# Optimization experiments

Measured on AMD Instinct MI355X. Metric: run time of the kernel, lower is better.

Reference implementation:

```python
import jax, jax.numpy as jnp
import numpy as np

GROUP = 16  # quantization group size along in_features
EPS = 1e-5


def setup_inputs() -> dict:
    key = jax.random.key(0)
    ks = jax.random.split(key, 6)
    B, D, L, R = 16384, 1024, 18, 32
    x = jax.random.normal(ks[0], (B, D), dtype=jnp.float32)
    # 4-bit codes in [0,16); shifted by -8 at dequant time -> values in [-8,7]
    wq = jax.random.randint(ks[1], (L, D, D), 0, 16, dtype=jnp.int32)
    # per-group positive scales, small so dequantized weights are O(0.1)
    scales = jax.random.uniform(ks[2], (L, D, D // GROUP), dtype=jnp.float32) * 0.05 + 0.005
    bias = jax.random.normal(ks[3], (L, D), dtype=jnp.float32) * 0.02
    # LoRA weights are zero-init in the module; use small random values so the
    # low-rank path is numerically exercised
    lora_a = jax.random.normal(ks[4], (L, R, D), dtype=jnp.float32) * 0.02
    lora_b = jax.random.normal(ks[5], (L, D, R), dtype=jnp.float32) * 0.02
    ln_gamma = jnp.ones((5, D), dtype=jnp.float32)
    ln_beta = jnp.zeros((5, D), dtype=jnp.float32)
    return {"x": x, "wq": wq, "scales": scales, "bias": bias,
            "lora_a": lora_a, "lora_b": lora_b,
            "ln_gamma": ln_gamma, "ln_beta": ln_beta}


def _dequant(wq_i, sc_i):
    # wq_i: [out, in] int codes; sc_i: [out, in//GROUP]
    O, I = wq_i.shape
    q = wq_i.astype(jnp.float32) - 8.0
    w = q.reshape(O, I // GROUP, GROUP) * sc_i[:, :, None]
    return w.reshape(O, I)


def _qlora(x, wq_i, sc_i, b_i, a_i, bm_i):
    w = _dequant(wq_i, sc_i)                       # [out, in]
    base = x @ w.T + b_i                           # frozen 4-bit base path
    lora = (x @ a_i.T) @ bm_i.T                    # low-rank adapter path
    return base + lora


def _layernorm(x, g, b):
    m = jnp.mean(x, axis=-1, keepdims=True)
    v = jnp.mean(jnp.square(x - m), axis=-1, keepdims=True)
    return (x - m) * jax.lax.rsqrt(v + EPS) * g + b


def reference(x, wq, scales, bias, lora_a, lora_b, ln_gamma, ln_beta):
    h = x
    for j in range(6):  # 6 residual blocks, 3 QLoRA layers each
        i = 3 * j
        r = h
        h = jax.nn.relu(_qlora(h, wq[i], scales[i], bias[i], lora_a[i], lora_b[i]))
        h = jax.nn.relu(_qlora(h, wq[i + 1], scales[i + 1], bias[i + 1], lora_a[i + 1], lora_b[i + 1]))
        h = _qlora(h, wq[i + 2], scales[i + 2], bias[i + 2], lora_a[i + 2], lora_b[i + 2])
        h = h + r
        if j < 5:
            h = _layernorm(h, ln_gamma[j], ln_beta[j])
    return h
```

## Files before the change

### kernel.cpp

```cpp
#include <hip/hip_runtime.h>
#include <hip/hip_bf16.h>
#include <stdint.h>

using bf16 = __hip_bfloat16;
typedef __attribute__((ext_vector_type(8))) short bf16x8;
typedef __attribute__((ext_vector_type(8))) unsigned short u16x8;
typedef __attribute__((ext_vector_type(16))) float f32x16;

#define B_ROWS 16384
#define D_DIM  1024
#define NLAYER 18

__device__ inline void gload_lds16(const bf16* g, bf16* l) {
    __builtin_amdgcn_global_load_lds(
        (const __attribute__((address_space(1))) void*)g,
        (__attribute__((address_space(3))) void*)l, 16, 0, 0);
}

__device__ inline unsigned short f2bf_bits(float f) {
    bf16 h = __float2bfloat16(f);
    return *reinterpret_cast<unsigned short*>(&h);
}
__device__ inline float bfbits2f(unsigned short u) {
    unsigned int x = ((unsigned int)u) << 16;
    return __uint_as_float(x);
}
__device__ inline void split_bf(float v, unsigned short& hi, unsigned short& lo) {
    hi = f2bf_bits(v);
    float hf = bfbits2f(hi);
    lo = f2bf_bits(v - hf);
}

__global__ __launch_bounds__(256)
void build_weff(const int* __restrict__ wq, const float* __restrict__ scales,
                const float* __restrict__ lora_a, const float* __restrict__ lora_b,
                bf16* __restrict__ weff_h, bf16* __restrict__ weff_l)
{
    const int bb = blockIdx.x;
    const int l  = bb >> 7;
    const int o0 = (bb & 127) * 8;
    __shared__ float bsh[8][32];
    {
        const int oo = threadIdx.x >> 5, rr = threadIdx.x & 31;
        bsh[oo][rr] = lora_b[((size_t)l * 1024 + o0 + oo) * 32 + rr];
    }
    __syncthreads();

    const float* abase = lora_a + (size_t)l * 32 * 1024;
    const int i0 = threadIdx.x * 4;
    float acc[8][4] = {};
    #pragma unroll 4
    for (int r = 0; r < 32; ++r) {
        float4 av = *reinterpret_cast<const float4*>(abase + (size_t)r * 1024 + i0);
        #pragma unroll
        for (int o = 0; o < 8; ++o) {
            const float br = bsh[o][r];
            acc[o][0] += br * av.x; acc[o][1] += br * av.y;
            acc[o][2] += br * av.z; acc[o][3] += br * av.w;
        }
    }
    #pragma unroll
    for (int o = 0; o < 8; ++o) {
        const size_t row = (size_t)l * 1024 + o0 + o;
        int4 q = *reinterpret_cast<const int4*>(wq + row * 1024 + i0);
        const float sc = scales[row * 64 + (i0 >> 4)];
        float w0 = (q.x - 8) * sc + acc[o][0];
        float w1 = (q.y - 8) * sc + acc[o][1];
        float w2 = (q.z - 8) * sc + acc[o][2];
        float w3 = (q.w - 8) * sc + acc[o][3];
        ushort4 uh, ul;
        split_bf(w0, uh.x, ul.x); split_bf(w1, uh.y, ul.y);
        split_bf(w2, uh.z, ul.z); split_bf(w3, uh.w, ul.w);
        *reinterpret_cast<ushort4*>(weff_h + row * 1024 + i0) = uh;
        *reinterpret_cast<ushort4*>(weff_l + row * 1024 + i0) = ul;
    }
}

__global__ __launch_bounds__(256)
void cast_split(const float* __restrict__ x, bf16* __restrict__ yh, bf16* __restrict__ yl)
{
    size_t i = ((size_t)blockIdx.x * 256 + threadIdx.x) * 4;
    float4 v = *reinterpret_cast<const float4*>(x + i);
    ushort4 uh, ul;
    split_bf(v.x, uh.x, ul.x); split_bf(v.y, uh.y, ul.y);
    split_bf(v.z, uh.z, ul.z); split_bf(v.w, uh.w, ul.w);
    *reinterpret_cast<ushort4*>(yh + i) = uh;
    *reinterpret_cast<ushort4*>(yl + i) = ul;
}

#define TILE_E 8192
#define SET_E  (4 * TILE_E)

#define SCHED0 __builtin_amdgcn_sched_barrier(0)

template<int MODE>
__global__ __launch_bounds__(512)
void qgemm3(const bf16* __restrict__ AH, const bf16* __restrict__ AL,
            const bf16* __restrict__ WH, const bf16* __restrict__ WL,
            const float* __restrict__ bias,
            const bf16* __restrict__ RH, const bf16* __restrict__ RL,
            bf16* __restrict__ OH, bf16* __restrict__ OL,
            float* __restrict__ Of)
{
    __shared__ bf16 smem[2 * SET_E];

    const int b  = blockIdx.x;
    const int sb = ((b & 7) << 5) | (b >> 3);
    const int n0 = (sb & 3) * 256;
    const int m0 = (sb >> 2) * 256;

    const int tid  = threadIdx.x;
    const int wave = tid >> 6;
    const int lane = tid & 63;
    const int wr = wave >> 2;
    const int wc = wave & 3;

    const int rl = lane >> 2;
    const int ps = lane & 3;
    const int l31 = lane & 31;
    const int khalf = lane >> 5;

    f32x16 acc[4][2] = {};

    auto stage = [&](int buf, int k0) {
        bf16* base = smem + buf * SET_E;
        #pragma unroll
        for (int t = 0; t < 2; ++t) {
            int s = wave * 2 + t;
            int r = s * 16 + rl;
            int q = ps ^ (r & 3) ^ ((r >> 2) & 3);
            size_t ga = (size_t)(m0 + r) * D_DIM + k0 + q * 8;
            size_t gb = (size_t)(n0 + r) * D_DIM + k0 + q * 8;
            bf16* dst = base + s * 512;
            gload_lds16(AH + ga, dst);
            gload_lds16(AL + ga, dst + TILE_E);
            gload_lds16(WH + gb, dst + 2 * TILE_E);
            gload_lds16(WL + gb, dst + 3 * TILE_E);
        }
    };

    stage(0, 0);

    #pragma unroll 1
    for (int kt = 0; kt < 32; ++kt) {
        const int cur = kt & 1;
        SCHED0;
        asm volatile("s_waitcnt vmcnt(0)" ::: "memory");
        SCHED0;
        __builtin_amdgcn_s_barrier();
        if (kt < 31)
            stage(cur ^ 1, (kt + 1) * 32);
        SCHED0;

        const bf16* tb = smem + cur * SET_E;
        bf16x8 wh[2][2], wl[2][2], ah[4][2], al[4][2];
        #pragma unroll
        for (int nt = 0; nt < 2; ++nt)
            #pragma unroll
            for (int kc = 0; kc < 2; ++kc) {
                int R = wc * 64 + nt * 32 + l31;
                int sl = kc * 2 + khalf;
                int p = sl ^ (R & 3) ^ ((R >> 2) & 3);
                int off = R * 32 + p * 8;
                wh[nt][kc] = *reinterpret_cast<const bf16x8*>(tb + 2 * TILE_E + off);
                wl[nt][kc] = *reinterpret_cast<const bf16x8*>(tb + 3 * TILE_E + off);
            }
        #pragma unroll
        for (int mt = 0; mt < 4; ++mt)
            #pragma unroll
            for (int kc = 0; kc < 2; ++kc) {
                int R = wr * 128 + mt * 32 + l31;
                int sl = kc * 2 + khalf;
                int p = sl ^ (R & 3) ^ ((R >> 2) & 3);
                int off = R * 32 + p * 8;
                ah[mt][kc] = *reinterpret_cast<const bf16x8*>(tb + off);
                al[mt][kc] = *reinterpret_cast<const bf16x8*>(tb + TILE_E + off);
            }

        __builtin_amdgcn_s_setprio(1);
        #pragma unroll
        for (int mt = 0; mt < 4; ++mt)
            #pragma unroll
            for (int nt = 0; nt < 2; ++nt)
                #pragma unroll
                for (int kc = 0; kc < 2; ++kc) {
                    acc[mt][nt] = __builtin_amdgcn_mfma_f32_32x32x16_bf16(ah[mt][kc], wh[nt][kc], acc[mt][nt], 0, 0, 0);
                    acc[mt][nt] = __builtin_amdgcn_mfma_f32_32x32x16_bf16(ah[mt][kc], wl[nt][kc], acc[mt][nt], 0, 0, 0);
                    acc[mt][nt] = __builtin_amdgcn_mfma_f32_32x32x16_bf16(al[mt][kc], wh[nt][kc], acc[mt][nt], 0, 0, 0);
                }
        __builtin_amdgcn_s_setprio(0);
    }

    SCHED0;
    asm volatile("s_waitcnt lgkmcnt(0)" ::: "memory");
    SCHED0;
    __builtin_amdgcn_s_barrier();

    float* cwave = reinterpret_cast<float*>(smem) + wave * 4096;
    const int rbase = 4 * khalf;
    const int rloc = lane >> 3;
    const int cloc = (lane & 7) * 8;

    #pragma unroll
    for (int half = 0; half < 2; ++half) {
        #pragma unroll
        for (int nt = 0; nt < 2; ++nt) {
            const float bv = bias[n0 + wc * 64 + nt * 32 + l31];
            const int lcol = nt * 32 + l31;
            const int chunk = lcol >> 2;
            #pragma unroll
            for (int mm = 0; mm < 2; ++mm) {
                const int mt = half * 2 + mm;
                #pragma unroll
                for (int reg = 0; reg < 16; ++reg) {
                    const int row32 = (reg & 3) + 8 * (reg >> 2) + rbase;
                    const int lrow = mm * 32 + row32;
                    float v = acc[mt][nt][reg] + bv;
                    if (MODE == 0) v = v > 0.f ? v : 0.f;
                    cwave[lrow * 64 + (chunk ^ (lrow & 15)) * 4 + (lcol & 3)] = v;
                }
            }
        }
        SCHED0;
        asm volatile("s_waitcnt lgkmcnt(0)" ::: "memory");
        SCHED0;

        #pragma unroll
        for (int pass = 0; pass < 8; ++pass) {
            const int lrow = pass * 8 + rloc;
            const int grow = m0 + wr * 128 + half * 64 + lrow;
            const size_t gbase = (size_t)grow * D_DIM + (n0 + wc * 64 + cloc);
            const int c0 = cloc >> 2;
            float4 v0 = *reinterpret_cast<const float4*>(&cwave[lrow * 64 + ((c0    ) ^ (lrow & 15)) * 4]);
            float4 v1 = *reinterpret_cast<const float4*>(&cwave[lrow * 64 + ((c0 + 1) ^ (lrow & 15)) * 4]);
            float vv[8] = {v0.x, v0.y, v0.z, v0.w, v1.x, v1.y, v1.z, v1.w};
            if (MODE != 0) {
                u16x8 rh = *reinterpret_cast<const u16x8*>(&RH[gbase]);
                u16x8 rl2 = *reinterpret_cast<const u16x8*>(&RL[gbase]);
                #pragma unroll
                for (int k = 0; k < 8; ++k)
                    vv[k] += bfbits2f(rh[k]) + bfbits2f(rl2[k]);
            }
            if (MODE == 2) {
                *reinterpret_cast<float4*>(&Of[gbase])     = make_float4(vv[0], vv[1], vv[2], vv[3]);
                *reinterpret_cast<float4*>(&Of[gbase + 4]) = make_float4(vv[4], vv[5], vv[6], vv[7]);
            } else {
                u16x8 ho, lo2;
                #pragma unroll
                for (int k = 0; k < 8; ++k) {
                    unsigned short h, l2;
                    split_bf(vv[k], h, l2);
                    ho[k] = h; lo2[k] = l2;
                }
                *reinterpret_cast<u16x8*>(&OH[gbase]) = ho;
                *reinterpret_cast<u16x8*>(&OL[gbase]) = lo2;
            }
        }
        SCHED0;
        asm volatile("s_waitcnt lgkmcnt(0)" ::: "memory");
        SCHED0;
    }
}

__global__ __launch_bounds__(256)
void ln_pair(const bf16* __restrict__ XH, const bf16* __restrict__ XL,
             bf16* __restrict__ YH, bf16* __restrict__ YL,
             const float* __restrict__ gamma, const float* __restrict__ beta)
{
    const int row = blockIdx.x;
    const int tid = threadIdx.x;
    const int lane = tid & 63;
    const int wave = tid >> 6;

    ushort4 uh = reinterpret_cast<const ushort4*>(XH + (size_t)row * D_DIM)[tid];
    ushort4 ul = reinterpret_cast<const ushort4*>(XL + (size_t)row * D_DIM)[tid];
    float v0 = bfbits2f(uh.x) + bfbits2f(ul.x);
    float v1 = bfbits2f(uh.y) + bfbits2f(ul.y);
    float v2 = bfbits2f(uh.z) + bfbits2f(ul.z);
    float v3 = bfbits2f(uh.w) + bfbits2f(ul.w);
    float s  = v0 + v1 + v2 + v3;
    float ss = v0 * v0 + v1 * v1 + v2 * v2 + v3 * v3;
    #pragma unroll
    for (int off = 32; off >= 1; off >>= 1) {
        s  += __shfl_xor(s, off, 64);
        ss += __shfl_xor(ss, off, 64);
    }
    __shared__ float red[8];
    if (lane == 0) { red[wave] = s; red[4 + wave] = ss; }
    __syncthreads();
    float S  = red[0] + red[1] + red[2] + red[3];
    float SS = red[4] + red[5] + red[6] + red[7];
    const float mean = S * (1.0f / D_DIM);
    const float var  = SS * (1.0f / D_DIM) - mean * mean;
    const float inv  = rsqrtf(var + 1e-5f);

    const int c0 = tid * 4;
    float y0 = (v0 - mean) * inv * gamma[c0 + 0] + beta[c0 + 0];
    float y1 = (v1 - mean) * inv * gamma[c0 + 1] + beta[c0 + 1];
    float y2 = (v2 - mean) * inv * gamma[c0 + 2] + beta[c0 + 2];
    float y3 = (v3 - mean) * inv * gamma[c0 + 3] + beta[c0 + 3];
    ushort4 oh, ol;
    split_bf(y0, oh.x, ol.x); split_bf(y1, oh.y, ol.y);
    split_bf(y2, oh.z, ol.z); split_bf(y3, oh.w, ol.w);
    reinterpret_cast<ushort4*>(YH + (size_t)row * D_DIM)[tid] = oh;
    reinterpret_cast<ushort4*>(YL + (size_t)row * D_DIM)[tid] = ol;
}

extern "C" void kernel_launch(void* const* d_in, const int* in_sizes, int n_in,
                              void* d_out, int out_size, void* d_ws, size_t ws_size,
                              hipStream_t stream)
{
    const float* x      = (const float*)d_in[0];
    const int*   wq     = (const int*)d_in[1];
    const float* scales = (const float*)d_in[2];
    const float* bias   = (const float*)d_in[3];
    const float* lora_a = (const float*)d_in[4];
    const float* lora_b = (const float*)d_in[5];
    const float* ln_g   = (const float*)d_in[6];
    const float* ln_b   = (const float*)d_in[7];
    float* out = (float*)d_out;

    char* ws = (char*)d_ws;
    const size_t W_ELEMS = (size_t)NLAYER * D_DIM * D_DIM;
    const size_t H_ELEMS = (size_t)B_ROWS * D_DIM;
    bf16* WHp = (bf16*)ws;
    bf16* WLp = WHp + W_ELEMS;
    bf16* HAh = WLp + W_ELEMS;
    bf16* HAl = HAh + H_ELEMS;
    bf16* HBh = HAl + H_ELEMS;
    bf16* HBl = HBh + H_ELEMS;
    bf16* HCh = (bf16*)d_out;
    bf16* HCl = HCh + H_ELEMS;

    build_weff<<<dim3(NLAYER * 128), dim3(256), 0, stream>>>(wq, scales, lora_a, lora_b, WHp, WLp);
    cast_split<<<dim3((B_ROWS * D_DIM) / (256 * 4)), dim3(256), 0, stream>>>(x, HAh, HAl);

    dim3 ggrid(256);
    for (int j = 0; j < 6; ++j) {
        const int l0 = 3 * j;
        const bf16* WH0 = WHp + (size_t)l0 * D_DIM * D_DIM;
        const bf16* WL0 = WLp + (size_t)l0 * D_DIM * D_DIM;
        const bf16* WH1 = WHp + (size_t)(l0 + 1) * D_DIM * D_DIM;
        const bf16* WL1 = WLp + (size_t)(l0 + 1) * D_DIM * D_DIM;
        const bf16* WH2 = WHp + (size_t)(l0 + 2) * D_DIM * D_DIM;
        const bf16* WL2 = WLp + (size_t)(l0 + 2) * D_DIM * D_DIM;
        const float* b0 = bias + (size_t)l0 * D_DIM;
        const float* b1 = bias + (size_t)(l0 + 1) * D_DIM;
        const float* b2 = bias + (size_t)(l0 + 2) * D_DIM;
        if (j < 5) {
            qgemm3<0><<<ggrid, 512, 0, stream>>>(HAh, HAl, WH0, WL0, b0, nullptr, nullptr, HBh, HBl, nullptr);
            qgemm3<0><<<ggrid, 512, 0, stream>>>(HBh, HBl, WH1, WL1, b1, nullptr, nullptr, HCh, HCl, nullptr);
            qgemm3<1><<<ggrid, 512, 0, stream>>>(HCh, HCl, WH2, WL2, b2, HAh, HAl, HBh, HBl, nullptr);
            ln_pair<<<dim3(B_ROWS), dim3(256), 0, stream>>>(HBh, HBl, HAh, HAl,
                                                            ln_g + (size_t)j * D_DIM, ln_b + (size_t)j * D_DIM);
        } else {
            qgemm3<0><<<ggrid, 512, 0, stream>>>(HAh, HAl, WH0, WL0, b0, nullptr, nullptr, HCh, HCl, nullptr);
            qgemm3<0><<<ggrid, 512, 0, stream>>>(HCh, HCl, WH1, WL1, b1, nullptr, nullptr, HBh, HBl, nullptr);
            qgemm3<2><<<ggrid, 512, 0, stream>>>(HBh, HBl, WH2, WL2, b2, HAh, HAl, nullptr, nullptr, out);
        }
    }
}
```

Baseline: 1.842 ms.

## Shrink GEMM tiles to 256x128 with K=16 steps and double the grid

Replaces the 256x256 tile with a K-step of 32 with a 256x128 tile and a K-step of 16, and launches 512 blocks instead of 256. Each wave now holds a 2x2 accumulator set instead of 4x2, and launch bounds request 4 waves per SIMD so more waves can be resident at once. The LDS staging layout is rebuilt with 32-row chunks and the XOR swizzle is removed, which may cause LDS bank conflicts. Smaller tiles lower reuse per byte loaded, and the loop now runs 64 iterations, so barrier and waitcnt overhead per FLOP roughly doubles.

```diff
diff --git a/kernel.cpp b/kernel.cpp
--- a/kernel.cpp
+++ b/kernel.cpp
@@ -88,13 +88,12 @@
     *reinterpret_cast<ushort4*>(yl + i) = ul;
 }
 
-#define TILE_E 8192
-#define SET_E  (4 * TILE_E)
+#define SET_E 12288
 
 #define SCHED0 __builtin_amdgcn_sched_barrier(0)
 
 template<int MODE>
-__global__ __launch_bounds__(512)
+__global__ __launch_bounds__(512, 4)
 void qgemm3(const bf16* __restrict__ AH, const bf16* __restrict__ AL,
             const bf16* __restrict__ WH, const bf16* __restrict__ WL,
             const float* __restrict__ bias,
@@ -102,92 +101,85 @@
             bf16* __restrict__ OH, bf16* __restrict__ OL,
             float* __restrict__ Of)
 {
-    __shared__ bf16 smem[2 * SET_E];
+    __shared__ __align__(16) char smem_raw[65536];
+    bf16* smem = reinterpret_cast<bf16*>(smem_raw);
 
     const int b  = blockIdx.x;
-    const int sb = ((b & 7) << 5) | (b >> 3);
-    const int n0 = (sb & 3) * 256;
-    const int m0 = (sb >> 2) * 256;
+    const int sb = ((b & 7) << 6) | (b >> 3);
+    const int n0 = (sb & 7) * 128;
+    const int m0 = (sb >> 3) * 256;
 
     const int tid  = threadIdx.x;
     const int wave = tid >> 6;
     const int lane = tid & 63;
-    const int wr = wave >> 2;
-    const int wc = wave & 3;
-
-    const int rl = lane >> 2;
-    const int ps = lane & 3;
+    const int wr = wave >> 1;
+    const int wc = wave & 1;
+
     const int l31 = lane & 31;
     const int khalf = lane >> 5;
-
-    f32x16 acc[4][2] = {};
+    const int srow = lane >> 1;
+    const int sslot = lane & 1;
+
+    f32x16 acc[2][2] = {};
 
     auto stage = [&](int buf, int k0) {
-        bf16* base = smem + buf * SET_E;
-        #pragma unroll
-        for (int t = 0; t < 2; ++t) {
-            int s = wave * 2 + t;
-            int r = s * 16 + rl;
-            int q = ps ^ (r & 3) ^ ((r >> 2) & 3);
-            size_t ga = (size_t)(m0 + r) * D_DIM + k0 + q * 8;
-            size_t gb = (size_t)(n0 + r) * D_DIM + k0 + q * 8;
-            bf16* dst = base + s * 512;
-            gload_lds16(AH + ga, dst);
-            gload_lds16(AL + ga, dst + TILE_E);
-            gload_lds16(WH + gb, dst + 2 * TILE_E);
-            gload_lds16(WL + gb, dst + 3 * TILE_E);
+        #pragma unroll
+        for (int j = 0; j < 3; ++j) {
+            const int cc = wave * 3 + j;
+            bf16* dst = smem + buf * SET_E + cc * 512;
+            if (cc < 8) {
+                size_t g = (size_t)(m0 + cc * 32 + srow) * D_DIM + k0 + sslot * 8;
+                gload_lds16(AH + g, dst);
+            } else if (cc < 16) {
+                size_t g = (size_t)(m0 + (cc - 8) * 32 + srow) * D_DIM + k0 + sslot * 8;
+                gload_lds16(AL + g, dst);
+            } else if (cc < 20) {
+                size_t g = (size_t)(n0 + (cc - 16) * 32 + srow) * D_DIM + k0 + sslot * 8;
+                gload_lds16(WH + g, dst);
+            } else {
+                size_t g = (size_t)(n0 + (cc - 20) * 32 + srow) * D_DIM + k0 + sslot * 8;
+                gload_lds16(WL + g, dst);
+            }
         }
     };
 
     stage(0, 0);
 
     #pragma unroll 1
-    for (int kt = 0; kt < 32; ++kt) {
+    for (int kt = 0; kt < 64; ++kt) {
         const int cur = kt & 1;
         SCHED0;
         asm volatile("s_waitcnt vmcnt(0)" ::: "memory");
         SCHED0;
         __builtin_amdgcn_s_barrier();
-        if (kt < 31)
-            stage(cur ^ 1, (kt + 1) * 32);
+        if (kt < 63)
+            stage(cur ^ 1, (kt + 1) * 16);
         SCHED0;
 
         const bf16* tb = smem + cur * SET_E;
-        bf16x8 wh[2][2], wl[2][2], ah[4][2], al[4][2];
-        #pragma unroll
-        for (int nt = 0; nt < 2; ++nt)
+        bf16x8 ah[2], al[2], wh[2], wl[2];
+        #pragma unroll
+        for (int nt = 0; nt < 2; ++nt) {
+            int off = (wc * 64 + nt * 32 + l31) * 16 + khalf * 8;
+            wh[nt] = *reinterpret_cast<const bf16x8*>(tb + 8192 + off);
+            wl[nt] = *reinterpret_cast<const bf16x8*>(tb + 10240 + off);
+        }
+        #pragma unroll
+        for (int mt = 0; mt < 2; ++mt) {
+            int off = (wr * 64 + mt * 32 + l31) * 16 + khalf * 8;
+            ah[mt] = *reinterpret_cast<const bf16x8*>(tb + off);
+            al[mt] = *reinterpret_cast<const bf16x8*>(tb + 4096 + off);
+        }
+
+        __builtin_amdgcn_s_setprio(1);
+        #pragma unroll
+        for (int mt = 0; mt < 2; ++mt)
             #pragma unroll
-            for (int kc = 0; kc < 2; ++kc) {
-                int R = wc * 64 + nt * 32 + l31;
-                int sl = kc * 2 + khalf;
-                int p = sl ^ (R & 3) ^ ((R >> 2) & 3);
-                int off = R * 32 + p * 8;
-                wh[nt][kc] = *reinterpret_cast<const bf16x8*>(tb + 2 * TILE_E + off);
-                wl[nt][kc] = *reinterpret_cast<const bf16x8*>(tb + 3 * TILE_E + off);
-            }
-        #pragma unroll
-        for (int mt = 0; mt < 4; ++mt)
-            #pragma unroll
-            for (int kc = 0; kc < 2; ++kc) {
-                int R = wr * 128 + mt * 32 + l31;
-                int sl = kc * 2 + khalf;
-                int p = sl ^ (R & 3) ^ ((R >> 2) & 3);
-                int off = R * 32 + p * 8;
-                ah[mt][kc] = *reinterpret_cast<const bf16x8*>(tb + off);
-                al[mt][kc] = *reinterpret_cast<const bf16x8*>(tb + TILE_E + off);
-            }
-
-        __builtin_amdgcn_s_setprio(1);
-        #pragma unroll
-        for (int mt = 0; mt < 4; ++mt)
-            #pragma unroll
-            for (int nt = 0; nt < 2; ++nt)
-                #pragma unroll
-                for (int kc = 0; kc < 2; ++kc) {
-                    acc[mt][nt] = __builtin_amdgcn_mfma_f32_32x32x16_bf16(ah[mt][kc], wh[nt][kc], acc[mt][nt], 0, 0, 0);
-                    acc[mt][nt] = __builtin_amdgcn_mfma_f32_32x32x16_bf16(ah[mt][kc], wl[nt][kc], acc[mt][nt], 0, 0, 0);
-                    acc[mt][nt] = __builtin_amdgcn_mfma_f32_32x32x16_bf16(al[mt][kc], wh[nt][kc], acc[mt][nt], 0, 0, 0);
-                }
+            for (int nt = 0; nt < 2; ++nt) {
+                acc[mt][nt] = __builtin_amdgcn_mfma_f32_32x32x16_bf16(ah[mt], wh[nt], acc[mt][nt], 0, 0, 0);
+                acc[mt][nt] = __builtin_amdgcn_mfma_f32_32x32x16_bf16(ah[mt], wl[nt], acc[mt][nt], 0, 0, 0);
+                acc[mt][nt] = __builtin_amdgcn_mfma_f32_32x32x16_bf16(al[mt], wh[nt], acc[mt][nt], 0, 0, 0);
+            }
         __builtin_amdgcn_s_setprio(0);
     }
 
@@ -196,29 +188,24 @@
     SCHED0;
     __builtin_amdgcn_s_barrier();
 
-    float* cwave = reinterpret_cast<float*>(smem) + wave * 4096;
+    float* cwave = reinterpret_cast<float*>(smem_raw) + wave * 2048;
     const int rbase = 4 * khalf;
     const int rloc = lane >> 3;
     const int cloc = (lane & 7) * 8;
 
     #pragma unroll
-    for (int half = 0; half < 2; ++half) {
+    for (int mt = 0; mt < 2; ++mt) {
         #pragma unroll
         for (int nt = 0; nt < 2; ++nt) {
             const float bv = bias[n0 + wc * 64 + nt * 32 + l31];
             const int lcol = nt * 32 + l31;
             const int chunk = lcol >> 2;
             #pragma unroll
-            for (int mm = 0; mm < 2; ++mm) {
-                const int mt = half * 2 + mm;
-                #pragma unroll
-                for (int reg = 0; reg < 16; ++reg) {
-                    const int row32 = (reg & 3) + 8 * (reg >> 2) + rbase;
-                    const int lrow = mm * 32 + row32;
-                    float v = acc[mt][nt][reg] + bv;
-                    if (MODE == 0) v = v > 0.f ? v : 0.f;
-                    cwave[lrow * 64 + (chunk ^ (lrow & 15)) * 4 + (lcol & 3)] = v;
-                }
+            for (int reg = 0; reg < 16; ++reg) {
+                const int row32 = (reg & 3) + 8 * (reg >> 2) + rbase;
+                float v = acc[mt][nt][reg] + bv;
+                if (MODE == 0) v = v > 0.f ? v : 0.f;
+                cwave[row32 * 64 + (chunk ^ (row32 & 15)) * 4 + (lcol & 3)] = v;
             }
         }
         SCHED0;
@@ -226,9 +213,9 @@
         SCHED0;
 
         #pragma unroll
-        for (int pass = 0; pass < 8; ++pass) {
+        for (int pass = 0; pass < 4; ++pass) {
             const int lrow = pass * 8 + rloc;
-            const int grow = m0 + wr * 128 + half * 64 + lrow;
+            const int grow = m0 + wr * 64 + mt * 32 + lrow;
             const size_t gbase = (size_t)grow * D_DIM + (n0 + wc * 64 + cloc);
             const int c0 = cloc >> 2;
             float4 v0 = *reinterpret_cast<const float4*>(&cwave[lrow * 64 + ((c0    ) ^ (lrow & 15)) * 4]);
@@ -335,7 +322,7 @@
     build_weff<<<dim3(NLAYER * 128), dim3(256), 0, stream>>>(wq, scales, lora_a, lora_b, WHp, WLp);
     cast_split<<<dim3((B_ROWS * D_DIM) / (256 * 4)), dim3(256), 0, stream>>>(x, HAh, HAl);
 
-    dim3 ggrid(256);
+    dim3 ggrid(512);
     for (int j = 0; j < 6; ++j) {
         const int l0 = 3 * j;
         const bf16* WH0 = WHp + (size_t)l0 * D_DIM * D_DIM;
```

New measurement: 2.297 ms. 24.7% more time.

## Deepen qgemm3 K pipeline to 4 stages with 16-wide K slices

Applied to the files above, without the earlier changes.

Replaces the 2-stage, 32-wide K double buffer with a 4-buffer ring of 16-wide K slices, keeping three loads in flight via partial vmcnt waits. The swizzled LDS layout is dropped for a plain row layout. The A fragment loads are split into two halves so half the MFMAs can start before the rest of A is read. This aims to hide global-load latency and overlap LDS reads with MFMA work. In exchange it doubles the barrier count, and the unswizzled 32-byte row stride may cause LDS bank conflicts.

```diff
diff --git a/kernel.cpp b/kernel.cpp
--- a/kernel.cpp
+++ b/kernel.cpp
@@ -88,8 +88,7 @@
     *reinterpret_cast<ushort4*>(yl + i) = ul;
 }
 
-#define TILE_E 8192
-#define SET_E  (4 * TILE_E)
+#define HB_E 16384
 
 #define SCHED0 __builtin_amdgcn_sched_barrier(0)
 
@@ -102,7 +101,7 @@
             bf16* __restrict__ OH, bf16* __restrict__ OL,
             float* __restrict__ Of)
 {
-    __shared__ bf16 smem[2 * SET_E];
+    __shared__ bf16 smem[4 * HB_E];
 
     const int b  = blockIdx.x;
     const int sb = ((b & 7) << 5) | (b >> 3);
@@ -115,79 +114,100 @@
     const int wr = wave >> 2;
     const int wc = wave & 3;
 
-    const int rl = lane >> 2;
-    const int ps = lane & 3;
     const int l31 = lane & 31;
     const int khalf = lane >> 5;
 
     f32x16 acc[4][2] = {};
 
-    auto stage = [&](int buf, int k0) {
-        bf16* base = smem + buf * SET_E;
-        #pragma unroll
-        for (int t = 0; t < 2; ++t) {
-            int s = wave * 2 + t;
-            int r = s * 16 + rl;
-            int q = ps ^ (r & 3) ^ ((r >> 2) & 3);
-            size_t ga = (size_t)(m0 + r) * D_DIM + k0 + q * 8;
-            size_t gb = (size_t)(n0 + r) * D_DIM + k0 + q * 8;
-            bf16* dst = base + s * 512;
-            gload_lds16(AH + ga, dst);
-            gload_lds16(AL + ga, dst + TILE_E);
-            gload_lds16(WH + gb, dst + 2 * TILE_E);
-            gload_lds16(WL + gb, dst + 3 * TILE_E);
-        }
+    const int srow = lane >> 1;
+    const int skl  = (lane & 1) * 8;
+    auto stage = [&](int hb, int h) {
+        bf16* base = smem + hb * HB_E + wave * 512;
+        const size_t kg = (size_t)h * 16 + skl;
+        const int rr = wave * 32 + srow;
+        gload_lds16(AH + (size_t)(m0 + rr) * D_DIM + kg, base);
+        gload_lds16(AL + (size_t)(m0 + rr) * D_DIM + kg, base + 4096);
+        gload_lds16(WH + (size_t)(n0 + rr) * D_DIM + kg, base + 8192);
+        gload_lds16(WL + (size_t)(n0 + rr) * D_DIM + kg, base + 12288);
     };
 
     stage(0, 0);
+    stage(1, 1);
+    stage(2, 2);
 
     #pragma unroll 1
-    for (int kt = 0; kt < 32; ++kt) {
-        const int cur = kt & 1;
-        SCHED0;
-        asm volatile("s_waitcnt vmcnt(0)" ::: "memory");
+    for (int h = 0; h < 64; ++h) {
+        SCHED0;
+        if (h < 62)      asm volatile("s_waitcnt vmcnt(8)" ::: "memory");
+        else if (h == 62) asm volatile("s_waitcnt vmcnt(4)" ::: "memory");
+        else              asm volatile("s_waitcnt vmcnt(0)" ::: "memory");
         SCHED0;
         __builtin_amdgcn_s_barrier();
-        if (kt < 31)
-            stage(cur ^ 1, (kt + 1) * 32);
-        SCHED0;
-
-        const bf16* tb = smem + cur * SET_E;
-        bf16x8 wh[2][2], wl[2][2], ah[4][2], al[4][2];
-        #pragma unroll
-        for (int nt = 0; nt < 2; ++nt)
-            #pragma unroll
-            for (int kc = 0; kc < 2; ++kc) {
-                int R = wc * 64 + nt * 32 + l31;
-                int sl = kc * 2 + khalf;
-                int p = sl ^ (R & 3) ^ ((R >> 2) & 3);
-                int off = R * 32 + p * 8;
-                wh[nt][kc] = *reinterpret_cast<const bf16x8*>(tb + 2 * TILE_E + off);
-                wl[nt][kc] = *reinterpret_cast<const bf16x8*>(tb + 3 * TILE_E + off);
-            }
-        #pragma unroll
-        for (int mt = 0; mt < 4; ++mt)
-            #pragma unroll
-            for (int kc = 0; kc < 2; ++kc) {
-                int R = wr * 128 + mt * 32 + l31;
-                int sl = kc * 2 + khalf;
-                int p = sl ^ (R & 3) ^ ((R >> 2) & 3);
-                int off = R * 32 + p * 8;
-                ah[mt][kc] = *reinterpret_cast<const bf16x8*>(tb + off);
-                al[mt][kc] = *reinterpret_cast<const bf16x8*>(tb + TILE_E + off);
-            }
-
+        if (h < 61)
+            stage((h + 3) & 3, h + 3);
+        SCHED0;
+
+        const bf16* tb = smem + (h & 3) * HB_E;
+
+        bf16x8 wfh[2], wfl[2], fah[4], fal[4];
+        #pragma unroll
+        for (int nt = 0; nt < 2; ++nt) {
+            int off = (wc * 64 + nt * 32 + l31) * 16 + khalf * 8;
+            wfh[nt] = *reinterpret_cast<const bf16x8*>(tb + 8192 + off);
+            wfl[nt] = *reinterpret_cast<const bf16x8*>(tb + 12288 + off);
+        }
+        #pragma unroll
+        for (int mt = 0; mt < 2; ++mt) {
+            int off = (wr * 128 + mt * 32 + l31) * 16 + khalf * 8;
+            fah[mt] = *reinterpret_cast<const bf16x8*>(tb + off);
+            fal[mt] = *reinterpret_cast<const bf16x8*>(tb + 4096 + off);
+        }
+        SCHED0;
+        asm volatile("s_waitcnt lgkmcnt(0)" ::: "memory");
+        SCHED0;
         __builtin_amdgcn_s_setprio(1);
         #pragma unroll
-        for (int mt = 0; mt < 4; ++mt)
-            #pragma unroll
-            for (int nt = 0; nt < 2; ++nt)
-                #pragma unroll
-                for (int kc = 0; kc < 2; ++kc) {
-                    acc[mt][nt] = __builtin_amdgcn_mfma_f32_32x32x16_bf16(ah[mt][kc], wh[nt][kc], acc[mt][nt], 0, 0, 0);
-                    acc[mt][nt] = __builtin_amdgcn_mfma_f32_32x32x16_bf16(ah[mt][kc], wl[nt][kc], acc[mt][nt], 0, 0, 0);
-                    acc[mt][nt] = __builtin_amdgcn_mfma_f32_32x32x16_bf16(al[mt][kc], wh[nt][kc], acc[mt][nt], 0, 0, 0);
-                }
+        for (int mt = 0; mt < 2; ++mt)
+            #pragma unroll
+            for (int nt = 0; nt < 2; ++nt)
+                acc[mt][nt] = __builtin_amdgcn_mfma_f32_32x32x16_bf16(fah[mt], wfh[nt], acc[mt][nt], 0, 0, 0);
+        #pragma unroll
+        for (int mt = 0; mt < 2; ++mt)
+            #pragma unroll
+            for (int nt = 0; nt < 2; ++nt)
+                acc[mt][nt] = __builtin_amdgcn_mfma_f32_32x32x16_bf16(fah[mt], wfl[nt], acc[mt][nt], 0, 0, 0);
+        #pragma unroll
+        for (int mt = 0; mt < 2; ++mt)
+            #pragma unroll
+            for (int nt = 0; nt < 2; ++nt)
+                acc[mt][nt] = __builtin_amdgcn_mfma_f32_32x32x16_bf16(fal[mt], wfh[nt], acc[mt][nt], 0, 0, 0);
+        __builtin_amdgcn_s_setprio(0);
+
+        #pragma unroll
+        for (int mt = 2; mt < 4; ++mt) {
+            int off = (wr * 128 + mt * 32 + l31) * 16 + khalf * 8;
+            fah[mt] = *reinterpret_cast<const bf16x8*>(tb + off);
+            fal[mt] = *reinterpret_cast<const bf16x8*>(tb + 4096 + off);
+        }
+        SCHED0;
+        asm volatile("s_waitcnt lgkmcnt(0)" ::: "memory");
+        SCHED0;
+        __builtin_amdgcn_s_setprio(1);
+        #pragma unroll
+        for (int mt = 2; mt < 4; ++mt)
+            #pragma unroll
+            for (int nt = 0; nt < 2; ++nt)
+                acc[mt][nt] = __builtin_amdgcn_mfma_f32_32x32x16_bf16(fah[mt], wfh[nt], acc[mt][nt], 0, 0, 0);
+        #pragma unroll
+        for (int mt = 2; mt < 4; ++mt)
+            #pragma unroll
+            for (int nt = 0; nt < 2; ++nt)
+                acc[mt][nt] = __builtin_amdgcn_mfma_f32_32x32x16_bf16(fah[mt], wfl[nt], acc[mt][nt], 0, 0, 0);
+        #pragma unroll
+        for (int mt = 2; mt < 4; ++mt)
+            #pragma unroll
+            for (int nt = 0; nt < 2; ++nt)
+                acc[mt][nt] = __builtin_amdgcn_mfma_f32_32x32x16_bf16(fal[mt], wfh[nt], acc[mt][nt], 0, 0, 0);
         __builtin_amdgcn_s_setprio(0);
     }
 
@@ -248,9 +268,9 @@
                 u16x8 ho, lo2;
                 #pragma unroll
                 for (int k = 0; k < 8; ++k) {
-                    unsigned short h, l2;
-                    split_bf(vv[k], h, l2);
-                    ho[k] = h; lo2[k] = l2;
+                    unsigned short hh, l2;
+                    split_bf(vv[k], hh, l2);
+                    ho[k] = hh; lo2[k] = l2;
                 }
                 *reinterpret_cast<u16x8*>(&OH[gbase]) = ho;
                 *reinterpret_cast<u16x8*>(&OL[gbase]) = lo2;
```

New measurement: 2.071 ms. 1.12x slower.
